# Optimization experiments

Measured on AMD Instinct MI355X. Metric: run time of the kernel, lower is better.

## Reference

```python
import jax, jax.numpy as jnp
import numpy as np

D_MODEL = 512
NHEAD = 8
HEAD_DIM = D_MODEL // NHEAD
DFF = 2048
RANK = 64
L = 1024
N = 8
EPS = 1e-5


def _layer_norm(x, g, b):
    m = jnp.mean(x, axis=-1, keepdims=True)
    v = jnp.mean(jnp.square(x - m), axis=-1, keepdims=True)
    return (x - m) * jax.lax.rsqrt(v + EPS) * g + b


def setup_inputs() -> dict:
    key = jax.random.key(0)
    ks = jax.random.split(key, 20)
    s = 1.0 / np.sqrt(D_MODEL)
    inp = {
        "q": jax.random.normal(ks[0], (L, N, D_MODEL), jnp.float32),
        "k": jax.random.normal(ks[1], (L, N, D_MODEL), jnp.float32),
        "v": jax.random.normal(ks[2], (L, N, D_MODEL), jnp.float32),
        # attention projections, stored (in, out) so x @ W
        "Wq": jax.random.normal(ks[3], (D_MODEL, D_MODEL), jnp.float32) * s,
        "bq": jnp.zeros((D_MODEL,), jnp.float32),
        "Wk": jax.random.normal(ks[4], (D_MODEL, D_MODEL), jnp.float32) * s,
        "bk": jnp.zeros((D_MODEL,), jnp.float32),
        "Wv": jax.random.normal(ks[5], (D_MODEL, D_MODEL), jnp.float32) * s,
        "bv": jnp.zeros((D_MODEL,), jnp.float32),
        "Wo": jax.random.normal(ks[6], (D_MODEL, D_MODEL), jnp.float32) * s,
        "bo": jnp.zeros((D_MODEL,), jnp.float32),
        "topk": jnp.float32(0.3),  # learned scalar, k = int(S * sigmoid(topk))
        "A1": jax.random.normal(ks[7], (D_MODEL, RANK), jnp.float32) * s,
        "B1": jax.random.normal(ks[8], (RANK, DFF), jnp.float32) / np.sqrt(RANK),
        "A2": jax.random.normal(ks[9], (DFF, RANK), jnp.float32) / np.sqrt(DFF),
        "B2": jax.random.normal(ks[10], (RANK, D_MODEL), jnp.float32) / np.sqrt(RANK),
        "g1": jnp.ones((D_MODEL,), jnp.float32),
        "be1": jnp.zeros((D_MODEL,), jnp.float32),
        "g2": jnp.ones((D_MODEL,), jnp.float32),
        "be2": jnp.zeros((D_MODEL,), jnp.float32),
    }
    return inp


def reference(q, k, v, Wq, bq, Wk, bk, Wv, bv, Wo, bo, topk,
              A1, B1, A2, B2, g1, be1, g2, be2):
    Lq, Nb, E = q.shape
    S = k.shape[0]
    H, Dh = NHEAD, HEAD_DIM

    # projections -> (N, L, H, Dh)
    qh = (q @ Wq + bq).reshape(Lq, Nb, H, Dh).transpose(1, 0, 2, 3)
    kh = (k @ Wk + bk).reshape(S, Nb, H, Dh).transpose(1, 0, 2, 3)
    vh = (v @ Wv + bv).reshape(S, Nb, H, Dh).transpose(1, 0, 2, 3)

    scores = jnp.einsum('nlhd,nshd->nlhs', qh, kh) / jnp.sqrt(jnp.float32(Dh))

    # dynamic top-k mask: keep the k = int(S * sigmoid(topk)) largest per row
    k_keep = (S * jax.nn.sigmoid(topk)).astype(jnp.int32)  # 588 for topk=0.3
    sorted_desc = jnp.sort(scores, axis=-1)[..., ::-1]
    idx = jnp.broadcast_to(k_keep - 1, scores.shape[:-1])[..., None]
    thresh = jnp.take_along_axis(sorted_desc, idx, axis=-1)  # k-th largest
    masked = jnp.where(scores >= thresh, scores, -jnp.inf)
    attn_w = jax.nn.softmax(masked, axis=-1)

    # note original flattens (d, h) order: 'nlhs,nshd->nldh' then view(L,N,E)
    ao = jnp.einsum('nlhs,nshd->nldh', attn_w, vh)
    ao = ao.transpose(1, 0, 2, 3).reshape(Lq, Nb, E)
    attn_out = ao @ Wo + bo

    src = _layer_norm(q + attn_out, g1, be1)
    ffn = jax.nn.relu(src @ A1 @ B1) @ A2 @ B2
    src = _layer_norm(src + ffn, g2, be2)
    return src
```

## Files before the change

kernel.cpp:

```cpp
#include <hip/hip_runtime.h>

typedef unsigned short u16;
typedef unsigned int u32;
typedef unsigned long long u64;
using s16x8 = __attribute__((ext_vector_type(8))) short;
using s16x4 = __attribute__((ext_vector_type(4))) short;
using u16x4 = __attribute__((ext_vector_type(4))) unsigned short;
using u32x4 = __attribute__((ext_vector_type(4))) unsigned int;
using f32x4 = __attribute__((ext_vector_type(4))) float;

__device__ __forceinline__ u16 f2bf(float f) {
  unsigned int u = __float_as_uint(f);
  u += 0x7FFFu + ((u >> 16) & 1u);
  return (u16)(u >> 16);
}
__device__ __forceinline__ float bf2f(u16 b) {
  return __uint_as_float(((u32)b) << 16);
}
__device__ __forceinline__ u32 pkbf(float a, float b) {
  u32 r;
  asm("v_cvt_pk_bf16_f32 %0, %1, %2" : "=v"(r) : "v"(a), "v"(b));
  return r;
}
__device__ __forceinline__ u64 cmp_ge(u32 key, u32 cand) {
  u64 m;
  asm("v_cmp_le_u32 %0, %1, %2" : "=s"(m) : "s"(cand), "v"(key));
  return m;
}
__device__ __forceinline__ u32 f2key(float f) {
  u32 u = __float_as_uint(f);
  u32 flip = (u32)((int)u >> 31) | 0x80000000u;
  return (u ^ flip) >> 16;
}
__device__ __forceinline__ float key2f(u32 k) {
  u32 t = k << 16;
  u32 msk = ((int)t < 0) ? 0x80000000u : 0xFFFF0000u;
  return __uint_as_float(t ^ msk);
}

__global__ __launch_bounds__(256) void prep_all(
    const float* __restrict__ q, const float* __restrict__ k, const float* __restrict__ v,
    const float* __restrict__ Wq, const float* __restrict__ Wk, const float* __restrict__ Wv,
    const float* __restrict__ Wo, const float* __restrict__ A1, const float* __restrict__ B1,
    const float* __restrict__ A2, const float* __restrict__ B2,
    u16* __restrict__ qb, u16* __restrict__ kb, u16* __restrict__ vb,
    u16* __restrict__ WqT, u16* __restrict__ WkT, u16* __restrict__ WvT, u16* __restrict__ WoT,
    u16* __restrict__ A1T, u16* __restrict__ B1T, u16* __restrict__ A2T, u16* __restrict__ B2T) {
  __shared__ u16 t[64][68];
  int b = blockIdx.x, tid = threadIdx.x;
  if (b < 12288) {
    const float* src = b < 4096 ? q : (b < 8192 ? k : v);
    u16* dst = b < 4096 ? qb : (b < 8192 ? kb : vb);
    int i = (b & 4095) * 256 + tid;
    float4 f = ((const float4*)src)[i];
    u16x4 o;
    o[0] = f2bf(f.x); o[1] = f2bf(f.y); o[2] = f2bf(f.z); o[3] = f2bf(f.w);
    ((u16x4*)dst)[i] = o;
    return;
  }
  b -= 12288;
  const float* src; u16* dst; int base, R, C;
  if (b < 64)        { src = Wq; dst = WqT; base = 0;   R = 512;  C = 512; }
  else if (b < 128)  { src = Wk; dst = WkT; base = 64;  R = 512;  C = 512; }
  else if (b < 192)  { src = Wv; dst = WvT; base = 128; R = 512;  C = 512; }
  else if (b < 256)  { src = Wo; dst = WoT; base = 192; R = 512;  C = 512; }
  else if (b < 264)  { src = A1; dst = A1T; base = 256; R = 512;  C = 64;  }
  else if (b < 296)  { src = B1; dst = B1T; base = 264; R = 64;   C = 2048;}
  else if (b < 328)  { src = A2; dst = A2T; base = 296; R = 2048; C = 64;  }
  else               { src = B2; dst = B2T; base = 328; R = 64;   C = 512; }
  int ti = b - base;
  int tpr = C >> 6;
  int r0 = (ti / tpr) * 64, c0 = (ti % tpr) * 64;
#pragma unroll
  for (int i = 0; i < 4; ++i) {
    int r = i * 16 + (tid >> 4), c = (tid & 15) * 4;
    float4 f = *(const float4*)&src[(size_t)(r0 + r) * C + c0 + c];
    t[r][c] = f2bf(f.x); t[r][c + 1] = f2bf(f.y);
    t[r][c + 2] = f2bf(f.z); t[r][c + 3] = f2bf(f.w);
  }
  __syncthreads();
#pragma unroll
  for (int i = 0; i < 4; ++i) {
    int cc = i * 16 + (tid >> 4), rr = (tid & 15) * 4;
    u16x4 o;
    o[0] = t[rr][cc]; o[1] = t[rr + 1][cc]; o[2] = t[rr + 2][cc]; o[3] = t[rr + 3][cc];
    *(u16x4*)&dst[(size_t)(c0 + cc) * R + r0 + rr] = o;
  }
}

__global__ __launch_bounds__(256, 4) void qkv_fused(
    const u16* __restrict__ qb, const u16* __restrict__ kb, const u16* __restrict__ vb,
    const u16* __restrict__ WqT, const u16* __restrict__ WkT, const u16* __restrict__ WvT,
    const float* __restrict__ bq, const float* __restrict__ bk, const float* __restrict__ bv,
    u16* __restrict__ Qw, u16* __restrict__ Kw, u16* __restrict__ Vw) {
  __shared__ __align__(16) u16 As[128][72];
  __shared__ __align__(16) u16 Bs[128][72];
  const int z = blockIdx.z;
  const u16* A = z == 0 ? qb : (z == 1 ? kb : vb);
  const u16* Bt = z == 0 ? WqT : (z == 1 ? WkT : WvT);
  const float* bias = z == 0 ? bq : (z == 1 ? bk : bv);
  u16* outp = z == 0 ? Qw : (z == 1 ? Kw : Vw);

  const int tid = threadIdx.x;
  const int m0 = blockIdx.y * 128, n0 = blockIdx.x * 128;
  const int lane = tid & 63, wid = tid >> 6;
  const int l16 = lane & 15, hi = lane >> 4;
  const int wr = (wid >> 1) * 64, wc = (wid & 1) * 64;

  f32x4 acc[4][4];
#pragma unroll
  for (int i = 0; i < 4; ++i)
#pragma unroll
    for (int j = 0; j < 4; ++j) acc[i][j] = (f32x4){0.f, 0.f, 0.f, 0.f};

  for (int k0 = 0; k0 < 512; k0 += 64) {
    if (k0) __syncthreads();
#pragma unroll
    for (int i = 0; i < 4; ++i) {
      int idx = i * 256 + tid;
      int r = idx >> 3, cc = (idx & 7) * 8;
      *(s16x8*)&As[r][cc] = *(const s16x8*)&A[(size_t)(m0 + r) * 512 + k0 + cc];
      *(s16x8*)&Bs[r][cc] = *(const s16x8*)&Bt[(size_t)(n0 + r) * 512 + k0 + cc];
    }
    __syncthreads();
#pragma unroll
    for (int kk = 0; kk < 2; ++kk) {
      const int kb_ = kk * 32 + hi * 8;
      s16x8 af[4], bf[4];
#pragma unroll
      for (int mf = 0; mf < 4; ++mf) af[mf] = *(const s16x8*)&As[wr + mf * 16 + l16][kb_];
#pragma unroll
      for (int nf = 0; nf < 4; ++nf) bf[nf] = *(const s16x8*)&Bs[wc + nf * 16 + l16][kb_];
#pragma unroll
      for (int mf = 0; mf < 4; ++mf)
#pragma unroll
        for (int nf = 0; nf < 4; ++nf)
          acc[mf][nf] = __builtin_amdgcn_mfma_f32_16x16x32_bf16(af[mf], bf[nf], acc[mf][nf], 0, 0, 0);
    }
  }

#pragma unroll
  for (int mf = 0; mf < 4; ++mf)
#pragma unroll
    for (int nf = 0; nf < 4; ++nf)
#pragma unroll
      for (int i = 0; i < 4; ++i) {
        int row = m0 + wr + mf * 16 + hi * 4 + i;
        int col = n0 + wc + nf * 16 + l16;
        float val = acc[mf][nf][i] + bias[col];
        if (z == 0) val *= 0.18033688f;
        int l = row >> 3, n = row & 7, hh = col >> 6, d = col & 63;
        if (z < 2)
          outp[(((size_t)(n * 8 + hh) * 1024 + l) << 6) + d] = f2bf(val);
        else
          outp[((size_t)(n * 8 + hh) * 64 + d) * 1024 + l] = f2bf(val);
      }
}

__global__ __launch_bounds__(512, 8) void attn_kernel(const u16* __restrict__ Qw,
                                                      const u16* __restrict__ Kw,
                                                      const u16* __restrict__ Vw,
                                                      const float* __restrict__ topk,
                                                      u16* __restrict__ ao) {
  __shared__ __align__(16) u16 scb[16 * 1024];
  __shared__ __align__(16) u16 Qt[16][72];
  __shared__ float invs[16];
  const int tid = threadIdx.x, lane = tid & 63, wid = tid >> 6;
  const int l16 = lane & 15, hi = lane >> 4;
  const int mb = blockIdx.x, nh = blockIdx.y;

  const int kkeep = (int)(1024.f / (1.f + __expf(-topk[0])));

  if (tid < 256) {
    int r = tid >> 4, dc = (tid & 15) << 2;
    *(s16x4*)&Qt[r][dc] =
        *(const s16x4*)&Qw[((size_t)nh * 1024 + mb * 16 + r) * 64 + dc];
  }
  __syncthreads();

  {
    const u16* Kb = Kw + (size_t)nh * 1024 * 64;
    s16x8 bq0 = *(const s16x8*)&Qt[l16][hi * 8];
    s16x8 bq1 = *(const s16x8*)&Qt[l16][32 + hi * 8];
    const int s0 = wid * 128;
    const size_t kbase = (size_t)(s0 + l16) * 64 + hi * 8;
    s16x8 c0 = *(const s16x8*)&Kb[kbase];
    s16x8 c1 = *(const s16x8*)&Kb[kbase + 32];
    char* rowq = (char*)scb + l16 * 2048;
    const int Xq = (l16 & 7) << 4;
#pragma unroll
    for (int nf = 0; nf < 8; ++nf) {
      s16x8 n0_, n1_;
      if (nf < 7) {
        const size_t nb = kbase + (size_t)(nf + 1) * 1024;
        n0_ = *(const s16x8*)&Kb[nb];
        n1_ = *(const s16x8*)&Kb[nb + 32];
      }
      f32x4 acc = {0.f, 0.f, 0.f, 0.f};
      acc = __builtin_amdgcn_mfma_f32_16x16x32_bf16(c0, bq0, acc, 0, 0, 0);
      acc = __builtin_amdgcn_mfma_f32_16x16x32_bf16(c1, bq1, acc, 0, 0, 0);
      u32 k0 = f2key(acc[0]) | (f2key(acc[1]) << 16);
      u32 k1 = f2key(acc[2]) | (f2key(acc[3]) << 16);
      int boff = (2 * (s0 + nf * 16 + 4 * hi)) ^ Xq;
      *(uint2*)(rowq + boff) = make_uint2(k0, k1);
      c0 = n0_; c1 = n1_;
    }
  }
  __syncthreads();

  {
    const int r0 = wid * 2, r1 = r0 + 1;
    char* rb0 = (char*)scb + r0 * 2048;
    char* rb1 = (char*)scb + r1 * 2048;
    const int X0 = (r0 & 7) << 4, X1 = (r1 & 7) << 4;
    const int o0 = (16 * lane) ^ X0, o0b = (16 * lane + 1024) ^ X0;
    const int o1 = (16 * lane) ^ X1, o1b = (16 * lane + 1024) ^ X1;
    u32x4 q0a = *(const u32x4*)(rb0 + o0), q0b = *(const u32x4*)(rb0 + o0b);
    u32x4 q1a = *(const u32x4*)(rb1 + o1), q1b = *(const u32x4*)(rb1 + o1b);
    u32 k0a[16], k1a[16];
#pragma unroll
    for (int j = 0; j < 4; ++j) {
      k0a[2 * j] = q0a[j] & 0xFFFFu; k0a[2 * j + 1] = q0a[j] >> 16;
      k0a[8 + 2 * j] = q0b[j] & 0xFFFFu; k0a[9 + 2 * j] = q0b[j] >> 16;
      k1a[2 * j] = q1a[j] & 0xFFFFu; k1a[2 * j + 1] = q1a[j] >> 16;
      k1a[8 + 2 * j] = q1b[j] & 0xFFFFu; k1a[9 + 2 * j] = q1b[j] >> 16;
    }
    u32 T0 = 0, T1 = 0;
    for (int bit = 15; bit >= 0; --bit) {
      const u32 bb = 1u << bit;
      u32 c0 = T0 + bb, c1 = T1 + bb;
      int n0 = 0, n1 = 0;
#pragma unroll
      for (int j = 0; j < 16; ++j) {
        n0 += __builtin_popcountll(cmp_ge(k0a[j], c0));
        n1 += __builtin_popcountll(cmp_ge(k1a[j], c1));
      }
      T0 = (n0 >= kkeep) ? c0 : T0;
      T1 = (n1 >= kkeep) ? c1 : T1;
    }
    const float tv0 = key2f(T0), tv1 = key2f(T1);
    float s0 = 0.f, s1 = 0.f;
    u32x4 w0a, w0b, w1a, w1b;
#pragma unroll
    for (int j = 0; j < 4; ++j) {
      {
        float e0 = (k0a[2 * j] >= T0) ? __builtin_amdgcn_exp2f(key2f(k0a[2 * j]) - tv0) : 0.f;
        float e1 = (k0a[2 * j + 1] >= T0) ? __builtin_amdgcn_exp2f(key2f(k0a[2 * j + 1]) - tv0) : 0.f;
        float e2 = (k0a[8 + 2 * j] >= T0) ? __builtin_amdgcn_exp2f(key2f(k0a[8 + 2 * j]) - tv0) : 0.f;
        float e3 = (k0a[9 + 2 * j] >= T0) ? __builtin_amdgcn_exp2f(key2f(k0a[9 + 2 * j]) - tv0) : 0.f;
        s0 += e0 + e1 + e2 + e3;
        w0a[j] = pkbf(e0, e1); w0b[j] = pkbf(e2, e3);
      }
      {
        float e0 = (k1a[2 * j] >= T1) ? __builtin_amdgcn_exp2f(key2f(k1a[2 * j]) - tv1) : 0.f;
        float e1 = (k1a[2 * j + 1] >= T1) ? __builtin_amdgcn_exp2f(key2f(k1a[2 * j + 1]) - tv1) : 0.f;
        float e2 = (k1a[8 + 2 * j] >= T1) ? __builtin_amdgcn_exp2f(key2f(k1a[8 + 2 * j]) - tv1) : 0.f;
        float e3 = (k1a[9 + 2 * j] >= T1) ? __builtin_amdgcn_exp2f(key2f(k1a[9 + 2 * j]) - tv1) : 0.f;
        s1 += e0 + e1 + e2 + e3;
        w1a[j] = pkbf(e0, e1); w1b[j] = pkbf(e2, e3);
      }
    }
    *(u32x4*)(rb0 + o0) = w0a; *(u32x4*)(rb0 + o0b) = w0b;
    *(u32x4*)(rb1 + o1) = w1a; *(u32x4*)(rb1 + o1b) = w1b;
#pragma unroll
    for (int off = 1; off < 64; off <<= 1) {
      s0 += __shfl_xor(s0, off);
      s1 += __shfl_xor(s1, off);
    }
    if (lane == 0) {
      invs[r0] = __builtin_amdgcn_rcpf(s0);
      invs[r1] = __builtin_amdgcn_rcpf(s1);
    }
  }
  __syncthreads();

  if (wid < 4) {
    const u16* Vb = Vw + (size_t)nh * 64 * 1024;
    const int d0 = wid * 16;
    f32x4 oacc0 = {0.f, 0.f, 0.f, 0.f};
    f32x4 oacc1 = {0.f, 0.f, 0.f, 0.f};
    const char* Pbase = (const char*)scb + l16 * 2048;
    const int Xp = (l16 & 7) << 4;
    const size_t vbase = (size_t)(d0 + l16) * 1024 + hi * 8;
    s16x8 v0 = *(const s16x8*)&Vb[vbase];
    s16x8 v1 = *(const s16x8*)&Vb[vbase + 32];
#pragma unroll
    for (int ks = 0; ks < 32; ks += 2) {
      s16x8 nv0, nv1;
      if (ks < 30) {
        nv0 = *(const s16x8*)&Vb[vbase + (size_t)(ks + 2) * 32];
        nv1 = *(const s16x8*)&Vb[vbase + (size_t)(ks + 3) * 32];
      }
      s16x8 a0 = *(const s16x8*)(Pbase + ((ks * 64 + hi * 16) ^ Xp));
      s16x8 a1 = *(const s16x8*)(Pbase + (((ks + 1) * 64 + hi * 16) ^ Xp));
      oacc0 = __builtin_amdgcn_mfma_f32_16x16x32_bf16(a0, v0, oacc0, 0, 0, 0);
      oacc1 = __builtin_amdgcn_mfma_f32_16x16x32_bf16(a1, v1, oacc1, 0, 0, 0);
      v0 = nv0; v1 = nv1;
    }
    const int n = nh >> 3, hh = nh & 7;
#pragma unroll
    for (int i = 0; i < 4; ++i) {
      int l = mb * 16 + hi * 4 + i;
      int d = d0 + l16;
      float vv = (oacc0[i] + oacc1[i]) * invs[hi * 4 + i];
      ao[(size_t)(l * 8 + n) * 512 + d * 8 + hh] = f2bf(vv);
    }
  }
}

template <bool FIRST>
__global__ __launch_bounds__(256, 2) void gemm_ln(const u16* __restrict__ A,
                                                  const u16* __restrict__ Bt,
                                                  const float* __restrict__ bias,
                                                  const float* __restrict__ residf,
                                                  const u16* __restrict__ residb,
                                                  const float* __restrict__ g,
                                                  const float* __restrict__ be,
                                                  float* __restrict__ outf,
                                                  u16* __restrict__ outb) {
  constexpr int K = FIRST ? 512 : 64;
  __shared__ __align__(16) u16 As[16][72];
  __shared__ float red_s[4][16];
  __shared__ float red_q[4][16];
  const int tid = threadIdx.x;
  const int lane = tid & 63, wid = tid >> 6;
  const int l16 = lane & 15, hi = lane >> 4;
  const int m0 = blockIdx.x * 16;
  const int wc = wid * 128;

  f32x4 acc[8];
#pragma unroll
  for (int nf = 0; nf < 8; ++nf) acc[nf] = (f32x4){0.f, 0.f, 0.f, 0.f};

  for (int k0 = 0; k0 < K; k0 += 64) {
    if (k0) __syncthreads();
    {
      int r = tid >> 4, c = (tid & 15) << 2;
      *(s16x4*)&As[r][c] = *(const s16x4*)&A[(size_t)(m0 + r) * K + k0 + c];
    }
    __syncthreads();
#pragma unroll
    for (int kk = 0; kk < 2; ++kk) {
      const int kb_ = kk * 32 + hi * 8;
      s16x8 a = *(const s16x8*)&As[l16][kb_];
#pragma unroll
      for (int nf = 0; nf < 8; ++nf) {
        s16x8 b = *(const s16x8*)&Bt[(size_t)(wc + nf * 16 + l16) * K + k0 + kb_];
        acc[nf] = __builtin_amdgcn_mfma_f32_16x16x32_bf16(a, b, acc[nf], 0, 0, 0);
      }
    }
  }

#pragma unroll
  for (int nf = 0; nf < 8; ++nf) {
    int col = wc + nf * 16 + l16;
#pragma unroll
    for (int i = 0; i < 4; ++i) {
      float v = acc[nf][i];
      int row = m0 + hi * 4 + i;
      if (FIRST) v += bias[col] + residf[(size_t)row * 512 + col];
      else v += bf2f(residb[(size_t)row * 512 + col]);
      acc[nf][i] = v;
    }
  }
  float s[4] = {0.f, 0.f, 0.f, 0.f}, q2[4] = {0.f, 0.f, 0.f, 0.f};
#pragma unroll
  for (int nf = 0; nf < 8; ++nf)
#pragma unroll
    for (int i = 0; i < 4; ++i) {
      s[i] += acc[nf][i];
      q2[i] += acc[nf][i] * acc[nf][i];
    }
#pragma unroll
  for (int i = 0; i < 4; ++i) {
#pragma unroll
    for (int off = 1; off < 16; off <<= 1) {
      s[i] += __shfl_xor(s[i], off);
      q2[i] += __shfl_xor(q2[i], off);
    }
  }
  if (l16 == 0) {
#pragma unroll
    for (int i = 0; i < 4; ++i) {
      red_s[wid][hi * 4 + i] = s[i];
      red_q[wid][hi * 4 + i] = q2[i];
    }
  }
  __syncthreads();
  float mean[4], rstd[4];
#pragma unroll
  for (int i = 0; i < 4; ++i) {
    int r = hi * 4 + i;
    float ms = red_s[0][r] + red_s[1][r] + red_s[2][r] + red_s[3][r];
    float mq = red_q[0][r] + red_q[1][r] + red_q[2][r] + red_q[3][r];
    mean[i] = ms * (1.f / 512.f);
    float var = mq * (1.f / 512.f) - mean[i] * mean[i];
    rstd[i] = rsqrtf(var + 1e-5f);
  }
#pragma unroll
  for (int nf = 0; nf < 8; ++nf) {
    int col = wc + nf * 16 + l16;
    float gv = g[col], bev = be[col];
#pragma unroll
    for (int i = 0; i < 4; ++i) {
      int row = m0 + hi * 4 + i;
      float y = (acc[nf][i] - mean[i]) * rstd[i] * gv + bev;
      if (FIRST) outb[(size_t)row * 512 + col] = f2bf(y);
      else outf[(size_t)row * 512 + col] = y;
    }
  }
}

__global__ __launch_bounds__(256, 4) void ffn3(const u16* __restrict__ srcb,
                                               const u16* __restrict__ A1T,
                                               const u16* __restrict__ B1T,
                                               const u16* __restrict__ A2T,
                                               u16* __restrict__ w2) {
  __shared__ __align__(16) u16 As[32][72];
  __shared__ __align__(16) u16 Bs[64][72];
  __shared__ __align__(16) u16 Us[32][72];
  __shared__ __align__(16) u16 B1s[64][72];
  __shared__ __align__(16) u16 A2s[64][72];
  __shared__ __align__(16) u16 Hs[32][72];
  const int tid = threadIdx.x;
  const int lane = tid & 63, wid = tid >> 6;
  const int l16 = lane & 15, hi = lane >> 4;
  const int m0 = blockIdx.x * 32;
  const int wm = (wid & 1) * 16, wn = (wid >> 1) * 32;

  f32x4 accu[2];
  accu[0] = (f32x4){0.f, 0.f, 0.f, 0.f};
  accu[1] = (f32x4){0.f, 0.f, 0.f, 0.f};
  for (int k0 = 0; k0 < 512; k0 += 64) {
    if (k0) __syncthreads();
    {
      int r = tid >> 3, c = (tid & 7) << 3;
      *(s16x8*)&As[r][c] = *(const s16x8*)&srcb[(size_t)(m0 + r) * 512 + k0 + c];
    }
#pragma unroll
    for (int i = 0; i < 2; ++i) {
      int idx = i * 256 + tid;
      int r = idx >> 3, c = (idx & 7) << 3;
      *(s16x8*)&Bs[r][c] = *(const s16x8*)&A1T[(size_t)r * 512 + k0 + c];
    }
    __syncthreads();
#pragma unroll
    for (int kk = 0; kk < 2; ++kk) {
      const int kb_ = kk * 32 + hi * 8;
      s16x8 a = *(const s16x8*)&As[wm + l16][kb_];
#pragma unroll
      for (int j = 0; j < 2; ++j) {
        s16x8 b = *(const s16x8*)&Bs[wn + j * 16 + l16][kb_];
        accu[j] = __builtin_amdgcn_mfma_f32_16x16x32_bf16(a, b, accu[j], 0, 0, 0);
      }
    }
  }
  __syncthreads();
#pragma unroll
  for (int j = 0; j < 2; ++j)
#pragma unroll
    for (int i = 0; i < 4; ++i)
      Us[wm + hi * 4 + i][wn + j * 16 + l16] = f2bf(accu[j][i]);

  f32x4 w2a[2];
  w2a[0] = (f32x4){0.f, 0.f, 0.f, 0.f};
  w2a[1] = (f32x4){0.f, 0.f, 0.f, 0.f};
  for (int jc = 0; jc < 32; ++jc) {
#pragma unroll
    for (int i = 0; i < 2; ++i) {
      int idx = i * 256 + tid;
      int r = idx >> 3, c = (idx & 7) << 3;
      *(s16x8*)&B1s[r][c] = *(const s16x8*)&B1T[(size_t)(jc * 64 + r) * 64 + c];
      *(s16x8*)&A2s[r][c] = *(const s16x8*)&A2T[(size_t)r * 2048 + jc * 64 + c];
    }
    __syncthreads();
    f32x4 ha[2];
    ha[0] = (f32x4){0.f, 0.f, 0.f, 0.f};
    ha[1] = (f32x4){0.f, 0.f, 0.f, 0.f};
#pragma unroll
    for (int kk = 0; kk < 2; ++kk) {
      const int kb_ = kk * 32 + hi * 8;
      s16x8 a = *(const s16x8*)&Us[wm + l16][kb_];
#pragma unroll
      for (int j = 0; j < 2; ++j) {
        s16x8 b = *(const s16x8*)&B1s[wn + j * 16 + l16][kb_];
        ha[j] = __builtin_amdgcn_mfma_f32_16x16x32_bf16(a, b, ha[j], 0, 0, 0);
      }
    }
#pragma unroll
    for (int j = 0; j < 2; ++j)
#pragma unroll
      for (int i = 0; i < 4; ++i)
        Hs[wm + hi * 4 + i][wn + j * 16 + l16] = f2bf(fmaxf(ha[j][i], 0.f));
    __syncthreads();
#pragma unroll
    for (int kk = 0; kk < 2; ++kk) {
      const int kb_ = kk * 32 + hi * 8;
      s16x8 a = *(const s16x8*)&Hs[wm + l16][kb_];
#pragma unroll
      for (int j = 0; j < 2; ++j) {
        s16x8 b = *(const s16x8*)&A2s[wn + j * 16 + l16][kb_];
        w2a[j] = __builtin_amdgcn_mfma_f32_16x16x32_bf16(a, b, w2a[j], 0, 0, 0);
      }
    }
    __syncthreads();
  }
#pragma unroll
  for (int j = 0; j < 2; ++j)
#pragma unroll
    for (int i = 0; i < 4; ++i)
      w2[(size_t)(m0 + wm + hi * 4 + i) * 64 + wn + j * 16 + l16] = f2bf(w2a[j][i]);
}

extern "C" void kernel_launch(void* const* d_in, const int* in_sizes, int n_in,
                              void* d_out, int out_size, void* d_ws, size_t ws_size,
                              hipStream_t stream) {
  const float* q = (const float*)d_in[0];
  const float* k = (const float*)d_in[1];
  const float* v = (const float*)d_in[2];
  const float* Wq = (const float*)d_in[3];
  const float* bq = (const float*)d_in[4];
  const float* Wk = (const float*)d_in[5];
  const float* bk = (const float*)d_in[6];
  const float* Wv = (const float*)d_in[7];
  const float* bv = (const float*)d_in[8];
  const float* Wo = (const float*)d_in[9];
  const float* bo = (const float*)d_in[10];
  const float* topk = (const float*)d_in[11];
  const float* A1 = (const float*)d_in[12];
  const float* B1 = (const float*)d_in[13];
  const float* A2 = (const float*)d_in[14];
  const float* B2 = (const float*)d_in[15];
  const float* g1 = (const float*)d_in[16];
  const float* be1 = (const float*)d_in[17];
  const float* g2 = (const float*)d_in[18];
  const float* be2 = (const float*)d_in[19];

  char* ws = (char*)d_ws;
  constexpr size_t SZ_TOK_BF = (size_t)8192 * 512 * 2;
  constexpr size_t SZ_W_BF = (size_t)512 * 512 * 2;
  constexpr size_t O_QB = 0;
  constexpr size_t O_KB = O_QB + SZ_TOK_BF;
  constexpr size_t O_VB = O_KB + SZ_TOK_BF;
  constexpr size_t O_QW = O_VB + SZ_TOK_BF;
  constexpr size_t O_KW = O_QW + SZ_TOK_BF;
  constexpr size_t O_VW = O_KW + SZ_TOK_BF;
  constexpr size_t O_WQT = O_VW + SZ_TOK_BF;
  constexpr size_t O_WKT = O_WQT + SZ_W_BF;
  constexpr size_t O_WVT = O_WKT + SZ_W_BF;
  constexpr size_t O_WOT = O_WVT + SZ_W_BF;
  constexpr size_t O_A1T = O_WOT + SZ_W_BF;
  constexpr size_t O_B1T = O_A1T + 65536;
  constexpr size_t O_A2T = O_B1T + 262144;
  constexpr size_t O_B2T = O_A2T + 262144;
  constexpr size_t O_AO = O_B2T + 65536;
  constexpr size_t O_SRCB = O_AO + SZ_TOK_BF;
  constexpr size_t O_W2 = O_SRCB + SZ_TOK_BF;

  u16* qb = (u16*)(ws + O_QB);
  u16* kb = (u16*)(ws + O_KB);
  u16* vb = (u16*)(ws + O_VB);
  u16* Qw_ = (u16*)(ws + O_QW);
  u16* Kw_ = (u16*)(ws + O_KW);
  u16* Vw_ = (u16*)(ws + O_VW);
  u16* WqT = (u16*)(ws + O_WQT);
  u16* WkT = (u16*)(ws + O_WKT);
  u16* WvT = (u16*)(ws + O_WVT);
  u16* WoT = (u16*)(ws + O_WOT);
  u16* A1T = (u16*)(ws + O_A1T);
  u16* B1T = (u16*)(ws + O_B1T);
  u16* A2T = (u16*)(ws + O_A2T);
  u16* B2T = (u16*)(ws + O_B2T);
  u16* ao = (u16*)(ws + O_AO);
  u16* srcb = (u16*)(ws + O_SRCB);
  u16* w2 = (u16*)(ws + O_W2);

  prep_all<<<12624, 256, 0, stream>>>(q, k, v, Wq, Wk, Wv, Wo, A1, B1, A2, B2,
                                      qb, kb, vb, WqT, WkT, WvT, WoT, A1T, B1T, A2T, B2T);

  qkv_fused<<<dim3(4, 64, 3), 256, 0, stream>>>(qb, kb, vb, WqT, WkT, WvT,
                                                bq, bk, bv, Qw_, Kw_, Vw_);

  attn_kernel<<<dim3(64, 64), 512, 0, stream>>>(Qw_, Kw_, Vw_, topk, ao);

  gemm_ln<true><<<512, 256, 0, stream>>>(ao, WoT, bo, q, nullptr, g1, be1, nullptr, srcb);

  ffn3<<<256, 256, 0, stream>>>(srcb, A1T, B1T, A2T, w2);

  gemm_ln<false><<<512, 256, 0, stream>>>(w2, B2T, nullptr, nullptr, srcb, g2, be2,
                                          (float*)d_out, nullptr);
}
```

Measured before the change: 287.0 us.

## Fuse fp32-to-bf16 activation conversion into QKV GEMM loads and relax attention bounds

Removes the separate pass that converted q, k and v to bf16 in a workspace. The QKV GEMM now reads fp32 inputs directly and packs them to bf16 while staging into shared memory, which drops one full write and re-read of three activation tensors. The GEMM then reads twice as many bytes per A tile, and each of the four N-tile blocks repeats the conversion. The attention kernel also lowers its launch-bounds occupancy hint from 8 to 4, stops unrolling the 16-step threshold bit search, and writes softmax probabilities to LDS as scalar stores instead of buffered vector stores, which is aimed at lowering register pressure.

```diff
diff --git a/kernel.cpp b/kernel.cpp
--- a/kernel.cpp
+++ b/kernel.cpp
@@ -38,27 +38,14 @@
   return __uint_as_float(t ^ msk);
 }
 
-__global__ __launch_bounds__(256) void prep_all(
-    const float* __restrict__ q, const float* __restrict__ k, const float* __restrict__ v,
+__global__ __launch_bounds__(256) void prep_w(
     const float* __restrict__ Wq, const float* __restrict__ Wk, const float* __restrict__ Wv,
     const float* __restrict__ Wo, const float* __restrict__ A1, const float* __restrict__ B1,
     const float* __restrict__ A2, const float* __restrict__ B2,
-    u16* __restrict__ qb, u16* __restrict__ kb, u16* __restrict__ vb,
     u16* __restrict__ WqT, u16* __restrict__ WkT, u16* __restrict__ WvT, u16* __restrict__ WoT,
     u16* __restrict__ A1T, u16* __restrict__ B1T, u16* __restrict__ A2T, u16* __restrict__ B2T) {
   __shared__ u16 t[64][68];
   int b = blockIdx.x, tid = threadIdx.x;
-  if (b < 12288) {
-    const float* src = b < 4096 ? q : (b < 8192 ? k : v);
-    u16* dst = b < 4096 ? qb : (b < 8192 ? kb : vb);
-    int i = (b & 4095) * 256 + tid;
-    float4 f = ((const float4*)src)[i];
-    u16x4 o;
-    o[0] = f2bf(f.x); o[1] = f2bf(f.y); o[2] = f2bf(f.z); o[3] = f2bf(f.w);
-    ((u16x4*)dst)[i] = o;
-    return;
-  }
-  b -= 12288;
   const float* src; u16* dst; int base, R, C;
   if (b < 64)        { src = Wq; dst = WqT; base = 0;   R = 512;  C = 512; }
   else if (b < 128)  { src = Wk; dst = WkT; base = 64;  R = 512;  C = 512; }
@@ -89,14 +76,14 @@
 }
 
 __global__ __launch_bounds__(256, 4) void qkv_fused(
-    const u16* __restrict__ qb, const u16* __restrict__ kb, const u16* __restrict__ vb,
+    const float* __restrict__ q, const float* __restrict__ k, const float* __restrict__ v,
     const u16* __restrict__ WqT, const u16* __restrict__ WkT, const u16* __restrict__ WvT,
     const float* __restrict__ bq, const float* __restrict__ bk, const float* __restrict__ bv,
     u16* __restrict__ Qw, u16* __restrict__ Kw, u16* __restrict__ Vw) {
   __shared__ __align__(16) u16 As[128][72];
   __shared__ __align__(16) u16 Bs[128][72];
   const int z = blockIdx.z;
-  const u16* A = z == 0 ? qb : (z == 1 ? kb : vb);
+  const float* A = z == 0 ? q : (z == 1 ? k : v);
   const u16* Bt = z == 0 ? WqT : (z == 1 ? WkT : WvT);
   const float* bias = z == 0 ? bq : (z == 1 ? bk : bv);
   u16* outp = z == 0 ? Qw : (z == 1 ? Kw : Vw);
@@ -119,7 +106,12 @@
     for (int i = 0; i < 4; ++i) {
       int idx = i * 256 + tid;
       int r = idx >> 3, cc = (idx & 7) * 8;
-      *(s16x8*)&As[r][cc] = *(const s16x8*)&A[(size_t)(m0 + r) * 512 + k0 + cc];
+      float4 f0 = *(const float4*)&A[(size_t)(m0 + r) * 512 + k0 + cc];
+      float4 f1 = *(const float4*)&A[(size_t)(m0 + r) * 512 + k0 + cc + 4];
+      u32x4 pk;
+      pk[0] = pkbf(f0.x, f0.y); pk[1] = pkbf(f0.z, f0.w);
+      pk[2] = pkbf(f1.x, f1.y); pk[3] = pkbf(f1.z, f1.w);
+      *(u32x4*)&As[r][cc] = pk;
       *(s16x8*)&Bs[r][cc] = *(const s16x8*)&Bt[(size_t)(n0 + r) * 512 + k0 + cc];
     }
     __syncthreads();
@@ -157,7 +149,7 @@
       }
 }
 
-__global__ __launch_bounds__(512, 8) void attn_kernel(const u16* __restrict__ Qw,
+__global__ __launch_bounds__(512, 4) void attn_kernel(const u16* __restrict__ Qw,
                                                       const u16* __restrict__ Kw,
                                                       const u16* __restrict__ Vw,
                                                       const float* __restrict__ topk,
@@ -226,6 +218,7 @@
       k1a[8 + 2 * j] = q1b[j] & 0xFFFFu; k1a[9 + 2 * j] = q1b[j] >> 16;
     }
     u32 T0 = 0, T1 = 0;
+#pragma unroll 1
     for (int bit = 15; bit >= 0; --bit) {
       const u32 bb = 1u << bit;
       u32 c0 = T0 + bb, c1 = T1 + bb;
@@ -240,7 +233,6 @@
     }
     const float tv0 = key2f(T0), tv1 = key2f(T1);
     float s0 = 0.f, s1 = 0.f;
-    u32x4 w0a, w0b, w1a, w1b;
 #pragma unroll
     for (int j = 0; j < 4; ++j) {
       {
@@ -249,7 +241,8 @@
         float e2 = (k0a[8 + 2 * j] >= T0) ? __builtin_amdgcn_exp2f(key2f(k0a[8 + 2 * j]) - tv0) : 0.f;
         float e3 = (k0a[9 + 2 * j] >= T0) ? __builtin_amdgcn_exp2f(key2f(k0a[9 + 2 * j]) - tv0) : 0.f;
         s0 += e0 + e1 + e2 + e3;
-        w0a[j] = pkbf(e0, e1); w0b[j] = pkbf(e2, e3);
+        *(u32*)(rb0 + o0 + 4 * j) = pkbf(e0, e1);
+        *(u32*)(rb0 + o0b + 4 * j) = pkbf(e2, e3);
       }
       {
         float e0 = (k1a[2 * j] >= T1) ? __builtin_amdgcn_exp2f(key2f(k1a[2 * j]) - tv1) : 0.f;
@@ -257,11 +250,10 @@
         float e2 = (k1a[8 + 2 * j] >= T1) ? __builtin_amdgcn_exp2f(key2f(k1a[8 + 2 * j]) - tv1) : 0.f;
         float e3 = (k1a[9 + 2 * j] >= T1) ? __builtin_amdgcn_exp2f(key2f(k1a[9 + 2 * j]) - tv1) : 0.f;
         s1 += e0 + e1 + e2 + e3;
-        w1a[j] = pkbf(e0, e1); w1b[j] = pkbf(e2, e3);
-      }
-    }
-    *(u32x4*)(rb0 + o0) = w0a; *(u32x4*)(rb0 + o0b) = w0b;
-    *(u32x4*)(rb1 + o1) = w1a; *(u32x4*)(rb1 + o1b) = w1b;
+        *(u32*)(rb1 + o1 + 4 * j) = pkbf(e0, e1);
+        *(u32*)(rb1 + o1b + 4 * j) = pkbf(e2, e3);
+      }
+    }
 #pragma unroll
     for (int off = 1; off < 64; off <<= 1) {
       s0 += __shfl_xor(s0, off);
@@ -539,10 +531,7 @@
   char* ws = (char*)d_ws;
   constexpr size_t SZ_TOK_BF = (size_t)8192 * 512 * 2;
   constexpr size_t SZ_W_BF = (size_t)512 * 512 * 2;
-  constexpr size_t O_QB = 0;
-  constexpr size_t O_KB = O_QB + SZ_TOK_BF;
-  constexpr size_t O_VB = O_KB + SZ_TOK_BF;
-  constexpr size_t O_QW = O_VB + SZ_TOK_BF;
+  constexpr size_t O_QW = 0;
   constexpr size_t O_KW = O_QW + SZ_TOK_BF;
   constexpr size_t O_VW = O_KW + SZ_TOK_BF;
   constexpr size_t O_WQT = O_VW + SZ_TOK_BF;
@@ -557,9 +546,6 @@
   constexpr size_t O_SRCB = O_AO + SZ_TOK_BF;
   constexpr size_t O_W2 = O_SRCB + SZ_TOK_BF;
 
-  u16* qb = (u16*)(ws + O_QB);
-  u16* kb = (u16*)(ws + O_KB);
-  u16* vb = (u16*)(ws + O_VB);
   u16* Qw_ = (u16*)(ws + O_QW);
   u16* Kw_ = (u16*)(ws + O_KW);
   u16* Vw_ = (u16*)(ws + O_VW);
@@ -575,10 +561,10 @@
   u16* srcb = (u16*)(ws + O_SRCB);
   u16* w2 = (u16*)(ws + O_W2);
 
-  prep_all<<<12624, 256, 0, stream>>>(q, k, v, Wq, Wk, Wv, Wo, A1, B1, A2, B2,
-                                      qb, kb, vb, WqT, WkT, WvT, WoT, A1T, B1T, A2T, B2T);
-
-  qkv_fused<<<dim3(4, 64, 3), 256, 0, stream>>>(qb, kb, vb, WqT, WkT, WvT,
+  prep_w<<<336, 256, 0, stream>>>(Wq, Wk, Wv, Wo, A1, B1, A2, B2,
+                                  WqT, WkT, WvT, WoT, A1T, B1T, A2T, B2T);
+
+  qkv_fused<<<dim3(4, 64, 3), 256, 0, stream>>>(q, k, v, WqT, WkT, WvT,
                                                 bq, bk, bv, Qw_, Kw_, Vw_);
 
   attn_kernel<<<dim3(64, 64), 512, 0, stream>>>(Qw_, Kw_, Vw_, topk, ao);
```

After: 269.3 us. 6.2% less time.
